# Kernel tuning notes

Hardware: AMD Instinct MI355X
Metric: run time of the kernel (lower is better)

## Reference

```python
import jax, jax.numpy as jnp
import numpy as np

N_NODE = 50000
N_EDGE = 600000
BATCH = 64
IN_DIM = 128
OUT_DIM = 128
ATTN_DIM = 128
N_REL_IDS = 2 * 237 + 1  # 475 relation embedding rows


def setup_inputs() -> dict:
    key = jax.random.key(0)
    ks = jax.random.split(key, 16)
    s = 1.0 / np.sqrt(IN_DIM)
    return {
        "q_sub": jax.random.randint(ks[0], (BATCH,), 0, N_NODE, dtype=jnp.int32),
        "q_rel": jax.random.randint(ks[1], (BATCH,), 0, N_REL_IDS, dtype=jnp.int32),
        "r_idx": jax.random.randint(ks[2], (N_EDGE,), 0, BATCH, dtype=jnp.int32),
        "hidden": jax.random.normal(ks[3], (N_NODE, IN_DIM), dtype=jnp.float32),
        "edge_sub": jax.random.randint(ks[4], (N_EDGE,), 0, N_NODE, dtype=jnp.int32),
        "edge_rel": jax.random.randint(ks[5], (N_EDGE,), 0, N_REL_IDS, dtype=jnp.int32),
        "edge_obj": jax.random.randint(ks[6], (N_EDGE,), 0, N_NODE, dtype=jnp.int32),
        "n_node": N_NODE,
        "rela_embed": jax.random.normal(ks[7], (N_REL_IDS, IN_DIM), dtype=jnp.float32),
        "Ws": jax.random.normal(ks[8], (IN_DIM, ATTN_DIM), dtype=jnp.float32) * s,
        "Wr": jax.random.normal(ks[9], (IN_DIM, ATTN_DIM), dtype=jnp.float32) * s,
        "Wqr_w": jax.random.normal(ks[10], (IN_DIM, ATTN_DIM), dtype=jnp.float32) * s,
        "Wqr_b": jax.random.normal(ks[11], (ATTN_DIM,), dtype=jnp.float32) * s,
        "wa_w": jax.random.normal(ks[12], (ATTN_DIM,), dtype=jnp.float32) * s,
        "wa_b": jax.random.normal(ks[13], (), dtype=jnp.float32) * s,
        "Wh": jax.random.normal(ks[14], (IN_DIM, OUT_DIM), dtype=jnp.float32) * s,
    }


def reference(q_sub, q_rel, r_idx, hidden, edge_sub, edge_rel, edge_obj, n_node,
              rela_embed, Ws, Wr, Wqr_w, Wqr_b, wa_w, wa_b, Wh):
    # gather: per-edge subject hidden state and relation embedding
    hs = hidden[edge_sub]            # [E, in_dim]
    hr = rela_embed[edge_rel]        # [E, in_dim]
    h_qr = rela_embed[q_rel][r_idx]  # [E, in_dim] query-relation embed per edge
    message = hs * hr                # [E, in_dim]
    # attention MLP: sigmoid(w_alpha(relu(Ws hs + Wr hr + Wqr h_qr + b)))
    pre = jax.nn.relu(hs @ Ws + hr @ Wr + h_qr @ Wqr_w + Wqr_b)  # [E, attn]
    alpha = jax.nn.sigmoid(pre @ wa_w + wa_b)                    # [E]
    message = alpha[:, None] * message
    # scatter-add into object node buckets
    message_agg = jax.ops.segment_sum(message, edge_obj, num_segments=n_node)  # [n_node, in_dim]
    # final linear, act = identity (default)
    return message_agg @ Wh
```

## Files before the change

kernel.cpp:

```cpp
#include <hip/hip_runtime.h>

typedef float f32x4 __attribute__((ext_vector_type(4)));
typedef _Float16 f16x8 __attribute__((ext_vector_type(8)));
typedef _Float16 v2h __attribute__((ext_vector_type(2)));
typedef short s16x2 __attribute__((ext_vector_type(2)));

__device__ __forceinline__ float hdot2(v2h a, v2h b, float c) {
#if __has_builtin(__builtin_amdgcn_fdot2)
  return __builtin_amdgcn_fdot2(a, b, c, false);
#else
  return c + (float)a[0] * (float)b[0] + (float)a[1] * (float)b[1];
#endif
}

__device__ __forceinline__ v2h relu2(v2h a) {
#if __has_builtin(__builtin_elementwise_max)
  const v2h z = {(_Float16)0, (_Float16)0};
  return __builtin_elementwise_max(a, z);
#else
  const v2h z = {(_Float16)0, (_Float16)0};
  s16x2 m = a > z;
  s16x2 bits = *(s16x2*)&a;
  s16x2 r = bits & m;
  return *(v2h*)&r;
#endif
}

__global__ __launch_bounds__(256) void conv_wr(
    const float* __restrict__ W0, const float* __restrict__ W1,
    const float* __restrict__ W2, const float* __restrict__ W3,
    _Float16* __restrict__ o0, _Float16* __restrict__ o1,
    _Float16* __restrict__ o2, _Float16* __restrict__ o3,
    const float* __restrict__ rela, _Float16* __restrict__ Rcat, int n_rel) {
  const int id = blockIdx.x * 256 + threadIdx.x;
  if (id < 65536) {
    const int m = id >> 14, e = id & 16383;
    const int k = e >> 7, c = e & 127;
    const float* W = (m == 0) ? W0 : (m == 1) ? W1 : (m == 2) ? W2 : W3;
    _Float16* o = (m == 0) ? o0 : (m == 1) ? o1 : (m == 2) ? o2 : o3;
    o[(k >> 3) * 1024 + c * 8 + (k & 7)] = (_Float16)W[e];
  } else {
    const int rid = id - 65536;
    if (rid < n_rel * 128)
      Rcat[(size_t)(rid >> 7) * 256 + (rid & 127)] = (_Float16)rela[rid];
  }
}

__global__ __launch_bounds__(256) void gemm_rel_dual(
    const _Float16* __restrict__ RcatA, const _Float16* __restrict__ Wrt8,
    const _Float16* __restrict__ Wqrt8, const float* __restrict__ bias,
    _Float16* __restrict__ RcatHi, _Float16* __restrict__ Rwqrt,
    int n_rel, int rel_blocks) {
  __shared__ _Float16 sW[16384];
  const bool second = (int)blockIdx.x >= rel_blocks;
  const int bb = second ? blockIdx.x - rel_blocks : blockIdx.x;
  const _Float16* Wt8 = second ? Wqrt8 : Wrt8;
  for (int i = threadIdx.x; i < 2048; i += 256)
    ((f32x4*)sW)[i] = ((const f32x4*)Wt8)[i];
  __syncthreads();

  const int wv = threadIdx.x >> 6, l = threadIdx.x & 63;
  const int row = bb * 64 + wv * 16 + (l & 15);
  const int kb = (l >> 4) * 8;
  const bool rvalid = row < n_rel;

  f16x8 a[4];
#pragma unroll
  for (int kk = 0; kk < 4; ++kk) {
    f16x8 t = {0, 0, 0, 0, 0, 0, 0, 0};
    if (rvalid) t = *(const f16x8*)(RcatA + (size_t)row * 256 + kb + 32 * kk);
    a[kk] = t;
  }

  f32x4 acc[8];
#pragma unroll
  for (int n = 0; n < 8; ++n) acc[n] = (f32x4){0.f, 0.f, 0.f, 0.f};
#pragma unroll
  for (int n = 0; n < 8; ++n)
#pragma unroll
    for (int kk = 0; kk < 4; ++kk) {
      const int kg = 4 * kk + (l >> 4);
      const f16x8 b = *(const f16x8*)(sW + kg * 1024 + (16 * n + (l & 15)) * 8);
      acc[n] = __builtin_amdgcn_mfma_f32_16x16x32_f16(a[kk], b, acc[n], 0, 0, 0);
    }

  const int orow_base = bb * 64 + wv * 16 + (l >> 4) * 4;
#pragma unroll
  for (int n = 0; n < 8; ++n) {
    const int col = 16 * n + (l & 15);
    const float badd = second ? bias[col] : 0.0f;
#pragma unroll
    for (int r4 = 0; r4 < 4; ++r4) {
      const int orow = orow_base + r4;
      if (orow < n_rel) {
        const float v = acc[n][r4] + badd;
        if (second) Rwqrt[(size_t)orow * 128 + col] = (_Float16)v;
        else        RcatHi[(size_t)orow * 256 + 128 + col] = (_Float16)v;
      }
    }
  }
}

__global__ __launch_bounds__(256) void gemm_hidden(
    const float* __restrict__ hidden, const _Float16* __restrict__ Wst8,
    _Float16* __restrict__ Hcat, int M) {
  __shared__ _Float16 sW[16384];
  for (int i = threadIdx.x; i < 2048; i += 256)
    ((f32x4*)sW)[i] = ((const f32x4*)Wst8)[i];
  __syncthreads();

  const int wv = threadIdx.x >> 6, l = threadIdx.x & 63;
  const int row = blockIdx.x * 64 + wv * 16 + (l & 15);
  const int kb = (l >> 4) * 8;
  const bool rvalid = row < M;

  f16x8 a[4];
#pragma unroll
  for (int kk = 0; kk < 4; ++kk) {
    f16x8 t = {0, 0, 0, 0, 0, 0, 0, 0};
    if (rvalid) {
      const f32x4 lo = *(const f32x4*)(hidden + (size_t)row * 128 + kb + 32 * kk);
      const f32x4 hi = *(const f32x4*)(hidden + (size_t)row * 128 + kb + 32 * kk + 4);
      t[0] = (_Float16)lo[0]; t[1] = (_Float16)lo[1];
      t[2] = (_Float16)lo[2]; t[3] = (_Float16)lo[3];
      t[4] = (_Float16)hi[0]; t[5] = (_Float16)hi[1];
      t[6] = (_Float16)hi[2]; t[7] = (_Float16)hi[3];
      *(f16x8*)(Hcat + (size_t)row * 256 + kb + 32 * kk) = t;
    }
    a[kk] = t;
  }

  f32x4 acc[8];
#pragma unroll
  for (int n = 0; n < 8; ++n) acc[n] = (f32x4){0.f, 0.f, 0.f, 0.f};
#pragma unroll
  for (int n = 0; n < 8; ++n)
#pragma unroll
    for (int kk = 0; kk < 4; ++kk) {
      const int kg = 4 * kk + (l >> 4);
      const f16x8 b = *(const f16x8*)(sW + kg * 1024 + (16 * n + (l & 15)) * 8);
      acc[n] = __builtin_amdgcn_mfma_f32_16x16x32_f16(a[kk], b, acc[n], 0, 0, 0);
    }

  const int orow_base = blockIdx.x * 64 + wv * 16 + (l >> 4) * 4;
#pragma unroll
  for (int n = 0; n < 8; ++n) {
    const int col = 16 * n + (l & 15);
#pragma unroll
    for (int r4 = 0; r4 < 4; ++r4) {
      const int orow = orow_base + r4;
      if (orow < M)
        Hcat[(size_t)orow * 256 + 128 + col] = (_Float16)acc[n][r4];
    }
  }
}

__global__ __launch_bounds__(256) void gemm_final(
    const _Float16* __restrict__ agg, const _Float16* __restrict__ Wht8,
    float* __restrict__ out, int M) {
  __shared__ _Float16 sW[16384];
  for (int i = threadIdx.x; i < 2048; i += 256)
    ((f32x4*)sW)[i] = ((const f32x4*)Wht8)[i];
  __syncthreads();

  const int wv = threadIdx.x >> 6, l = threadIdx.x & 63;
  const int row = blockIdx.x * 64 + wv * 16 + (l & 15);
  const int kb = (l >> 4) * 8;
  const bool rvalid = row < M;

  f16x8 a[4];
#pragma unroll
  for (int kk = 0; kk < 4; ++kk) {
    f16x8 t = {0, 0, 0, 0, 0, 0, 0, 0};
    if (rvalid) t = *(const f16x8*)(agg + (size_t)row * 128 + kb + 32 * kk);
    a[kk] = t;
  }

  f32x4 acc[8];
#pragma unroll
  for (int n = 0; n < 8; ++n) acc[n] = (f32x4){0.f, 0.f, 0.f, 0.f};
#pragma unroll
  for (int n = 0; n < 8; ++n)
#pragma unroll
    for (int kk = 0; kk < 4; ++kk) {
      const int kg = 4 * kk + (l >> 4);
      const f16x8 b = *(const f16x8*)(sW + kg * 1024 + (16 * n + (l & 15)) * 8);
      acc[n] = __builtin_amdgcn_mfma_f32_16x16x32_f16(a[kk], b, acc[n], 0, 0, 0);
    }

  const int orow_base = blockIdx.x * 64 + wv * 16 + (l >> 4) * 4;
#pragma unroll
  for (int n = 0; n < 8; ++n) {
    const int col = 16 * n + (l & 15);
#pragma unroll
    for (int r4 = 0; r4 < 4; ++r4) {
      const int orow = orow_base + r4;
      if (orow < M) out[(size_t)orow * 128 + col] = acc[n][r4];
    }
  }
}

__global__ __launch_bounds__(256) void hist_kernel(const int* __restrict__ edge_obj,
                                                   int* __restrict__ deg, int E) {
  for (int i = blockIdx.x * blockDim.x + threadIdx.x; i < E; i += gridDim.x * blockDim.x)
    atomicAdd(deg + edge_obj[i], 1);
}

__global__ __launch_bounds__(256) void scan_pass1(const int* __restrict__ deg,
                                                  int* __restrict__ bsum, int n) {
  const int b = blockIdx.x, t = threadIdx.x;
  const int i0 = b * 512 + t, i1 = i0 + 256;
  int v = 0;
  if (i0 < n) v += deg[i0];
  if (i1 < n) v += deg[i1];
  __shared__ int s[256];
  s[t] = v;
  __syncthreads();
  for (int o = 128; o > 0; o >>= 1) {
    if (t < o) s[t] += s[t + o];
    __syncthreads();
  }
  if (t == 0) bsum[b] = s[0];
}

__global__ __launch_bounds__(1024) void scan_pass2(const int* __restrict__ bsum,
                                                   int* __restrict__ bbase,
                                                   int* __restrict__ off,
                                                   int nb, int n) {
  const int t = threadIdx.x;
  __shared__ int s[1024];
  const int v = (t < nb) ? bsum[t] : 0;
  s[t] = v;
  __syncthreads();
  for (int o = 1; o < 1024; o <<= 1) {
    const int a = (t >= o) ? s[t - o] : 0;
    __syncthreads();
    s[t] += a;
    __syncthreads();
  }
  if (t < nb) bbase[t] = s[t] - v;
  if (t == 1023) off[n] = s[1023];
}

__global__ __launch_bounds__(256) void scan_pass3(const int* __restrict__ deg,
                                                  const int* __restrict__ bbase,
                                                  int* __restrict__ off,
                                                  int* __restrict__ cursor, int n) {
  const int b = blockIdx.x, t = threadIdx.x;
  const int i0 = b * 512 + t, i1 = i0 + 256;
  const int d0 = (i0 < n) ? deg[i0] : 0;
  const int d1 = (i1 < n) ? deg[i1] : 0;
  __shared__ int s[512];
  s[t] = d0;
  s[t + 256] = d1;
  __syncthreads();
  for (int o = 1; o < 512; o <<= 1) {
    const int a0 = (t >= o) ? s[t - o] : 0;
    const int a1 = (t + 256 >= o) ? s[t + 256 - o] : 0;
    __syncthreads();
    s[t] += a0;
    s[t + 256] += a1;
    __syncthreads();
  }
  const int base = bbase[b];
  if (i0 < n) { const int e = base + s[t] - d0;       off[i0] = e; cursor[i0] = e; }
  if (i1 < n) { const int e = base + s[t + 256] - d1; off[i1] = e; cursor[i1] = e; }
}

__global__ __launch_bounds__(256) void scatter_kernel(
    const int* __restrict__ edge_obj, const int* __restrict__ edge_sub,
    const int* __restrict__ edge_rel, const int* __restrict__ r_idx,
    const int* __restrict__ q_rel, int* __restrict__ cursor,
    int2* __restrict__ ssrq, int E) {
  for (int i = blockIdx.x * blockDim.x + threadIdx.x; i < E; i += gridDim.x * blockDim.x) {
    const int p = atomicAdd(cursor + edge_obj[i], 1);
    ssrq[p] = make_int2(edge_sub[i], (edge_rel[i] << 9) | q_rel[r_idx[i]]);
  }
}

__global__ __launch_bounds__(256) void reduce_f16(
    const int2* __restrict__ ssrq, const int* __restrict__ offs,
    const _Float16* __restrict__ Hcat, const _Float16* __restrict__ Rcat,
    const _Float16* __restrict__ Rwqrt, const float* __restrict__ wa_w,
    const float* __restrict__ wa_b_p, _Float16* __restrict__ agg, int n_node) {
  const int node = (blockIdx.x * blockDim.x + threadIdx.x) >> 6;
  if (node >= n_node) return;
  const int l = threadIdx.x & 63;
  const int g = l >> 4;
  const int d0 = (l & 15) * 8;

  v2h wa2[4];
  {
    const float4 w0 = *(const float4*)(wa_w + d0);
    const float4 w1 = *(const float4*)(wa_w + d0 + 4);
    wa2[0] = (v2h){(_Float16)w0.x, (_Float16)w0.y};
    wa2[1] = (v2h){(_Float16)w0.z, (_Float16)w0.w};
    wa2[2] = (v2h){(_Float16)w1.x, (_Float16)w1.y};
    wa2[3] = (v2h){(_Float16)w1.z, (_Float16)w1.w};
  }
  const float wab = wa_b_p[0];

  const int start = offs[node], end = offs[node + 1];
  v2h acc2[4] = {};

  for (int base = start; base < end; base += 64) {
    const int cnt = min(end - base, 64);
    int s_all = 0, rq_all = 0;
    if (l < cnt) { const int2 sr = ssrq[base + l]; s_all = sr.x; rq_all = sr.y; }
    for (int c = 0; c < cnt; c += 4) {
      const int src = c + g;
      const bool valid = src < cnt;
      const int sv = __shfl(s_all, src);
      const int rqv = __shfl(rq_all, src);
      const int rv = rqv >> 9, qv = rqv & 511;

      f32x4 rw = *(const f32x4*)(Hcat + ((size_t)sv << 8) + 128 + d0);
      f32x4 rr = *(const f32x4*)(Rcat + ((size_t)rv << 8) + 128 + d0);
      f32x4 rq = *(const f32x4*)(Rwqrt + ((size_t)qv << 7) + d0);
      f32x4 rh = *(const f32x4*)(Hcat + ((size_t)sv << 8) + d0);
      f32x4 rg = *(const f32x4*)(Rcat + ((size_t)rv << 8) + d0);
      const v2h* hw = (const v2h*)&rw;
      const v2h* hr_ = (const v2h*)&rr;
      const v2h* hq = (const v2h*)&rq;
      const v2h* hh = (const v2h*)&rh;
      const v2h* hg = (const v2h*)&rg;

      float part = 0.0f;
      v2h prod[4];
#pragma unroll
      for (int i = 0; i < 4; ++i) {
        const v2h pre = relu2(hw[i] + hr_[i] + hq[i]);
        part = hdot2(pre, wa2[i], part);
        prod[i] = hh[i] * hg[i];
      }
      part += __shfl_xor(part, 1);
      part += __shfl_xor(part, 2);
      part += __shfl_xor(part, 4);
      part += __shfl_xor(part, 8);
      const float alpha = valid ? 1.0f / (1.0f + __expf(-(part + wab))) : 0.0f;
      const _Float16 ah = (_Float16)alpha;
      const v2h alpha2 = {ah, ah};
#pragma unroll
      for (int i = 0; i < 4; ++i) acc2[i] += alpha2 * prod[i];
    }
  }

#pragma unroll
  for (int i = 0; i < 4; ++i) {
    unsigned x = *(unsigned*)&acc2[i];
    unsigned y = (unsigned)__shfl_xor((int)x, 16);
    acc2[i] += *(v2h*)&y;
    x = *(unsigned*)&acc2[i];
    y = (unsigned)__shfl_xor((int)x, 32);
    acc2[i] += *(v2h*)&y;
  }
  if (l < 16)
    *(f32x4*)(agg + (size_t)node * 128 + d0) = *(f32x4*)acc2;
}

extern "C" void kernel_launch(void* const* d_in, const int* in_sizes, int n_in,
                              void* d_out, int out_size, void* d_ws, size_t ws_size,
                              hipStream_t stream) {
  const int* q_rel = (const int*)d_in[1];
  const int* r_idx = (const int*)d_in[2];
  const float* hidden = (const float*)d_in[3];
  const int* edge_sub = (const int*)d_in[4];
  const int* edge_rel = (const int*)d_in[5];
  const int* edge_obj = (const int*)d_in[6];
  const float* rela = (const float*)d_in[8];
  const float* Ws = (const float*)d_in[9];
  const float* Wr = (const float*)d_in[10];
  const float* Wqr_w = (const float*)d_in[11];
  const float* Wqr_b = (const float*)d_in[12];
  const float* wa_w = (const float*)d_in[13];
  const float* wa_b = (const float*)d_in[14];
  const float* Wh = (const float*)d_in[15];

  const int E = in_sizes[2];
  const int n_node = in_sizes[3] / 128;
  const int n_rel = in_sizes[8] / 128;
  float* out = (float*)d_out;

  auto al = [](size_t x) { return (x + 511) & ~(size_t)511; };
  char* ws = (char*)d_ws;
  size_t o = 0;
  _Float16* Hcat = (_Float16*)(ws + o);  o += al((size_t)n_node * 256 * 2);
  _Float16* agg  = (_Float16*)(ws + o);  o += al((size_t)n_node * 128 * 2);
  _Float16* Rcat = (_Float16*)(ws + o);  o += al((size_t)n_rel * 256 * 2);
  _Float16* Rwqrt = (_Float16*)(ws + o); o += al((size_t)n_rel * 128 * 2);
  _Float16* Wst8 = (_Float16*)(ws + o);  o += al(16384 * 2);
  _Float16* Wrt8 = (_Float16*)(ws + o);  o += al(16384 * 2);
  _Float16* Wqrt8 = (_Float16*)(ws + o); o += al(16384 * 2);
  _Float16* Wht8 = (_Float16*)(ws + o);  o += al(16384 * 2);
  int* deg = (int*)(ws + o);       o += al((size_t)n_node * 4);
  int* offs = (int*)(ws + o);      o += al((size_t)(n_node + 1) * 4);
  int* curs = (int*)(ws + o);      o += al((size_t)n_node * 4);
  int* bsum = (int*)(ws + o);      o += al(1024 * 4);
  int* bbase = (int*)(ws + o);     o += al(1024 * 4);
  int2* ssrq = (int2*)(ws + o);    o += al((size_t)E * 8);

  (void)hipMemsetAsync(deg, 0, (size_t)n_node * 4, stream);
  hist_kernel<<<dim3(1024), dim3(256), 0, stream>>>(edge_obj, deg, E);
  const int nb = (n_node + 511) / 512;
  scan_pass1<<<dim3(nb), dim3(256), 0, stream>>>(deg, bsum, n_node);
  scan_pass2<<<dim3(1), dim3(1024), 0, stream>>>(bsum, bbase, offs, nb, n_node);
  scan_pass3<<<dim3(nb), dim3(256), 0, stream>>>(deg, bbase, offs, curs, n_node);
  scatter_kernel<<<dim3(1024), dim3(256), 0, stream>>>(
      edge_obj, edge_sub, edge_rel, r_idx, q_rel, curs, ssrq, E);

  const int prep_ids = 65536 + n_rel * 128;
  conv_wr<<<dim3((prep_ids + 255) / 256), dim3(256), 0, stream>>>(
      Ws, Wr, Wqr_w, Wh, Wst8, Wrt8, Wqrt8, Wht8, rela, Rcat, n_rel);

  const int rel_blocks = (n_rel + 63) / 64;
  gemm_rel_dual<<<dim3(rel_blocks * 2), dim3(256), 0, stream>>>(
      Rcat, Wrt8, Wqrt8, Wqr_b, Rcat, Rwqrt, n_rel, rel_blocks);

  const int node_blocks = (n_node + 63) / 64;
  gemm_hidden<<<dim3(node_blocks), dim3(256), 0, stream>>>(hidden, Wst8, Hcat, n_node);

  const int rblocks = (n_node * 64 + 255) / 256;
  reduce_f16<<<dim3(rblocks), dim3(256), 0, stream>>>(
      ssrq, offs, Hcat, Rcat, Rwqrt, wa_w, wa_b, agg, n_node);

  gemm_final<<<dim3(node_blocks), dim3(256), 0, stream>>>(agg, Wht8, out, n_node);
}
```

Measured before the change: 259.3 us.

## Merge sort pipeline into one cooperative kernel and fuse weight prep into GEMMs

Replaces the memset, histogram, three scan passes and scatter with a single cooperative kernel separated by grid-wide syncs. The weight fp32-to-fp16 conversion and relation GEMMs are folded into one prep_gemm launch that converts weights into shared memory per block, and gemm_final converts Wh itself. The aim is to cut the launch count and the intermediate weight buffers. In exchange, every block now redoes the weight conversion, and the grid syncs add latency; the block-level scan now covers at most 256 partial sums instead of 1024.

```diff
diff --git a/kernel.cpp b/kernel.cpp
--- a/kernel.cpp
+++ b/kernel.cpp
@@ -1,4 +1,7 @@
 #include <hip/hip_runtime.h>
+#include <hip/hip_cooperative_groups.h>
+
+namespace cg = cooperative_groups;
 
 typedef float f32x4 __attribute__((ext_vector_type(4)));
 typedef _Float16 f16x8 __attribute__((ext_vector_type(8)));
@@ -26,49 +29,131 @@
 #endif
 }
 
-__global__ __launch_bounds__(256) void conv_wr(
-    const float* __restrict__ W0, const float* __restrict__ W1,
-    const float* __restrict__ W2, const float* __restrict__ W3,
-    _Float16* __restrict__ o0, _Float16* __restrict__ o1,
-    _Float16* __restrict__ o2, _Float16* __restrict__ o3,
-    const float* __restrict__ rela, _Float16* __restrict__ Rcat, int n_rel) {
-  const int id = blockIdx.x * 256 + threadIdx.x;
-  if (id < 65536) {
-    const int m = id >> 14, e = id & 16383;
-    const int k = e >> 7, c = e & 127;
-    const float* W = (m == 0) ? W0 : (m == 1) ? W1 : (m == 2) ? W2 : W3;
-    _Float16* o = (m == 0) ? o0 : (m == 1) ? o1 : (m == 2) ? o2 : o3;
-    o[(k >> 3) * 1024 + c * 8 + (k & 7)] = (_Float16)W[e];
+__global__ __launch_bounds__(256, 4) void sort_coop(
+    const int* __restrict__ edge_obj, const int* __restrict__ edge_sub,
+    const int* __restrict__ edge_rel, const int* __restrict__ r_idx,
+    const int* __restrict__ q_rel, int* deg, int* bsum, int* bbase,
+    int* offs, int* curs, int2* ssrq, int E, int n, int nb) {
+  cg::grid_group grid = cg::this_grid();
+  __shared__ int s[512];
+  const int tid = blockIdx.x * 256 + threadIdx.x;
+  const int nthr = gridDim.x * 256;
+  const int t = threadIdx.x;
+  const int b = blockIdx.x;
+
+  for (int i = tid; i < n; i += nthr) deg[i] = 0;
+  grid.sync();
+
+  for (int i = tid; i < E; i += nthr) atomicAdd(&deg[edge_obj[i]], 1);
+  grid.sync();
+
+  if (b < nb) {
+    const int i0 = b * 512 + t, i1 = i0 + 256;
+    int v = 0;
+    if (i0 < n) v += deg[i0];
+    if (i1 < n) v += deg[i1];
+    s[t] = v;
+    __syncthreads();
+    for (int o = 128; o > 0; o >>= 1) {
+      if (t < o) s[t] += s[t + o];
+      __syncthreads();
+    }
+    if (t == 0) bsum[b] = s[0];
+  }
+  grid.sync();
+
+  if (b == 0) {
+    const int v = (t < nb) ? bsum[t] : 0;
+    s[t] = v;
+    __syncthreads();
+    for (int o = 1; o < 256; o <<= 1) {
+      const int a = (t >= o) ? s[t - o] : 0;
+      __syncthreads();
+      s[t] += a;
+      __syncthreads();
+    }
+    if (t < nb) bbase[t] = s[t] - v;
+    if (t == 255) offs[n] = s[255];
+  }
+  grid.sync();
+
+  if (b < nb) {
+    const int i0 = b * 512 + t, i1 = i0 + 256;
+    const int d0 = (i0 < n) ? deg[i0] : 0;
+    const int d1 = (i1 < n) ? deg[i1] : 0;
+    s[t] = d0;
+    s[t + 256] = d1;
+    __syncthreads();
+    for (int o = 1; o < 512; o <<= 1) {
+      const int a0 = (t >= o) ? s[t - o] : 0;
+      const int a1 = (t + 256 >= o) ? s[t + 256 - o] : 0;
+      __syncthreads();
+      s[t] += a0;
+      s[t + 256] += a1;
+      __syncthreads();
+    }
+    const int base = bbase[b];
+    if (i0 < n) { const int e = base + s[t] - d0;       offs[i0] = e; curs[i0] = e; }
+    if (i1 < n) { const int e = base + s[t + 256] - d1; offs[i1] = e; curs[i1] = e; }
+  }
+  grid.sync();
+
+  for (int i = tid; i < E; i += nthr) {
+    const int p = atomicAdd(&curs[edge_obj[i]], 1);
+    ssrq[p] = make_int2(edge_sub[i], (edge_rel[i] << 9) | q_rel[r_idx[i]]);
+  }
+}
+
+__global__ __launch_bounds__(256) void prep_gemm(
+    const float* __restrict__ hidden, const float* __restrict__ rela,
+    const float* __restrict__ Ws, const float* __restrict__ Wr,
+    const float* __restrict__ Wqr, const float* __restrict__ Wqr_b,
+    _Float16* __restrict__ Hcat, _Float16* __restrict__ Rcat,
+    _Float16* __restrict__ Rwqrt, int n_node, int n_rel,
+    int hid_blocks, int rel_blocks) {
+  __shared__ _Float16 sW[16384];
+  const int bidx = blockIdx.x;
+  const float* A;
+  const float* W;
+  const float* bias = nullptr;
+  _Float16* Lo = nullptr;
+  _Float16* Chi;
+  int M, bb, ldc, coff;
+  if (bidx < hid_blocks) {
+    bb = bidx; A = hidden; W = Ws; Lo = Hcat; Chi = Hcat;
+    M = n_node; ldc = 256; coff = 128;
+  } else if (bidx < hid_blocks + rel_blocks) {
+    bb = bidx - hid_blocks; A = rela; W = Wr; Lo = Rcat; Chi = Rcat;
+    M = n_rel; ldc = 256; coff = 128;
   } else {
-    const int rid = id - 65536;
-    if (rid < n_rel * 128)
-      Rcat[(size_t)(rid >> 7) * 256 + (rid & 127)] = (_Float16)rela[rid];
-  }
-}
-
-__global__ __launch_bounds__(256) void gemm_rel_dual(
-    const _Float16* __restrict__ RcatA, const _Float16* __restrict__ Wrt8,
-    const _Float16* __restrict__ Wqrt8, const float* __restrict__ bias,
-    _Float16* __restrict__ RcatHi, _Float16* __restrict__ Rwqrt,
-    int n_rel, int rel_blocks) {
-  __shared__ _Float16 sW[16384];
-  const bool second = (int)blockIdx.x >= rel_blocks;
-  const int bb = second ? blockIdx.x - rel_blocks : blockIdx.x;
-  const _Float16* Wt8 = second ? Wqrt8 : Wrt8;
-  for (int i = threadIdx.x; i < 2048; i += 256)
-    ((f32x4*)sW)[i] = ((const f32x4*)Wt8)[i];
+    bb = bidx - hid_blocks - rel_blocks; A = rela; W = Wqr; Chi = Rwqrt;
+    bias = Wqr_b; M = n_rel; ldc = 128; coff = 0;
+  }
+
+  for (int i = threadIdx.x; i < 16384; i += 256) {
+    const int k = i >> 7, c = i & 127;
+    sW[(k >> 3) * 1024 + c * 8 + (k & 7)] = (_Float16)W[i];
+  }
   __syncthreads();
 
   const int wv = threadIdx.x >> 6, l = threadIdx.x & 63;
   const int row = bb * 64 + wv * 16 + (l & 15);
   const int kb = (l >> 4) * 8;
-  const bool rvalid = row < n_rel;
+  const bool rvalid = row < M;
 
   f16x8 a[4];
 #pragma unroll
   for (int kk = 0; kk < 4; ++kk) {
     f16x8 t = {0, 0, 0, 0, 0, 0, 0, 0};
-    if (rvalid) t = *(const f16x8*)(RcatA + (size_t)row * 256 + kb + 32 * kk);
+    if (rvalid) {
+      const f32x4 lo = *(const f32x4*)(A + (size_t)row * 128 + kb + 32 * kk);
+      const f32x4 hi = *(const f32x4*)(A + (size_t)row * 128 + kb + 32 * kk + 4);
+      t[0] = (_Float16)lo[0]; t[1] = (_Float16)lo[1];
+      t[2] = (_Float16)lo[2]; t[3] = (_Float16)lo[3];
+      t[4] = (_Float16)hi[0]; t[5] = (_Float16)hi[1];
+      t[6] = (_Float16)hi[2]; t[7] = (_Float16)hi[3];
+      if (Lo) *(f16x8*)(Lo + (size_t)row * 256 + kb + 32 * kk) = t;
+    }
     a[kk] = t;
   }
 
@@ -80,33 +165,32 @@
 #pragma unroll
     for (int kk = 0; kk < 4; ++kk) {
       const int kg = 4 * kk + (l >> 4);
-      const f16x8 b = *(const f16x8*)(sW + kg * 1024 + (16 * n + (l & 15)) * 8);
-      acc[n] = __builtin_amdgcn_mfma_f32_16x16x32_f16(a[kk], b, acc[n], 0, 0, 0);
+      const f16x8 bfrag = *(const f16x8*)(sW + kg * 1024 + (16 * n + (l & 15)) * 8);
+      acc[n] = __builtin_amdgcn_mfma_f32_16x16x32_f16(a[kk], bfrag, acc[n], 0, 0, 0);
     }
 
   const int orow_base = bb * 64 + wv * 16 + (l >> 4) * 4;
 #pragma unroll
   for (int n = 0; n < 8; ++n) {
     const int col = 16 * n + (l & 15);
-    const float badd = second ? bias[col] : 0.0f;
+    const float badd = bias ? bias[col] : 0.0f;
 #pragma unroll
     for (int r4 = 0; r4 < 4; ++r4) {
       const int orow = orow_base + r4;
-      if (orow < n_rel) {
-        const float v = acc[n][r4] + badd;
-        if (second) Rwqrt[(size_t)orow * 128 + col] = (_Float16)v;
-        else        RcatHi[(size_t)orow * 256 + 128 + col] = (_Float16)v;
-      }
-    }
-  }
-}
-
-__global__ __launch_bounds__(256) void gemm_hidden(
-    const float* __restrict__ hidden, const _Float16* __restrict__ Wst8,
-    _Float16* __restrict__ Hcat, int M) {
+      if (orow < M)
+        Chi[(size_t)orow * ldc + coff + col] = (_Float16)(acc[n][r4] + badd);
+    }
+  }
+}
+
+__global__ __launch_bounds__(256) void gemm_final(
+    const _Float16* __restrict__ agg, const float* __restrict__ Wh,
+    float* __restrict__ out, int M) {
   __shared__ _Float16 sW[16384];
-  for (int i = threadIdx.x; i < 2048; i += 256)
-    ((f32x4*)sW)[i] = ((const f32x4*)Wst8)[i];
+  for (int i = threadIdx.x; i < 16384; i += 256) {
+    const int k = i >> 7, c = i & 127;
+    sW[(k >> 3) * 1024 + c * 8 + (k & 7)] = (_Float16)Wh[i];
+  }
   __syncthreads();
 
   const int wv = threadIdx.x >> 6, l = threadIdx.x & 63;
@@ -118,15 +202,7 @@
 #pragma unroll
   for (int kk = 0; kk < 4; ++kk) {
     f16x8 t = {0, 0, 0, 0, 0, 0, 0, 0};
-    if (rvalid) {
-      const f32x4 lo = *(const f32x4*)(hidden + (size_t)row * 128 + kb + 32 * kk);
-      const f32x4 hi = *(const f32x4*)(hidden + (size_t)row * 128 + kb + 32 * kk + 4);
-      t[0] = (_Float16)lo[0]; t[1] = (_Float16)lo[1];
-      t[2] = (_Float16)lo[2]; t[3] = (_Float16)lo[3];
-      t[4] = (_Float16)hi[0]; t[5] = (_Float16)hi[1];
-      t[6] = (_Float16)hi[2]; t[7] = (_Float16)hi[3];
-      *(f16x8*)(Hcat + (size_t)row * 256 + kb + 32 * kk) = t;
-    }
+    if (rvalid) t = *(const f16x8*)(agg + (size_t)row * 128 + kb + 32 * kk);
     a[kk] = t;
   }
 
@@ -138,54 +214,8 @@
 #pragma unroll
     for (int kk = 0; kk < 4; ++kk) {
       const int kg = 4 * kk + (l >> 4);
-      const f16x8 b = *(const f16x8*)(sW + kg * 1024 + (16 * n + (l & 15)) * 8);
-      acc[n] = __builtin_amdgcn_mfma_f32_16x16x32_f16(a[kk], b, acc[n], 0, 0, 0);
-    }
-
-  const int orow_base = blockIdx.x * 64 + wv * 16 + (l >> 4) * 4;
-#pragma unroll
-  for (int n = 0; n < 8; ++n) {
-    const int col = 16 * n + (l & 15);
-#pragma unroll
-    for (int r4 = 0; r4 < 4; ++r4) {
-      const int orow = orow_base + r4;
-      if (orow < M)
-        Hcat[(size_t)orow * 256 + 128 + col] = (_Float16)acc[n][r4];
-    }
-  }
-}
-
-__global__ __launch_bounds__(256) void gemm_final(
-    const _Float16* __restrict__ agg, const _Float16* __restrict__ Wht8,
-    float* __restrict__ out, int M) {
-  __shared__ _Float16 sW[16384];
-  for (int i = threadIdx.x; i < 2048; i += 256)
-    ((f32x4*)sW)[i] = ((const f32x4*)Wht8)[i];
-  __syncthreads();
-
-  const int wv = threadIdx.x >> 6, l = threadIdx.x & 63;
-  const int row = blockIdx.x * 64 + wv * 16 + (l & 15);
-  const int kb = (l >> 4) * 8;
-  const bool rvalid = row < M;
-
-  f16x8 a[4];
-#pragma unroll
-  for (int kk = 0; kk < 4; ++kk) {
-    f16x8 t = {0, 0, 0, 0, 0, 0, 0, 0};
-    if (rvalid) t = *(const f16x8*)(agg + (size_t)row * 128 + kb + 32 * kk);
-    a[kk] = t;
-  }
-
-  f32x4 acc[8];
-#pragma unroll
-  for (int n = 0; n < 8; ++n) acc[n] = (f32x4){0.f, 0.f, 0.f, 0.f};
-#pragma unroll
-  for (int n = 0; n < 8; ++n)
-#pragma unroll
-    for (int kk = 0; kk < 4; ++kk) {
-      const int kg = 4 * kk + (l >> 4);
-      const f16x8 b = *(const f16x8*)(sW + kg * 1024 + (16 * n + (l & 15)) * 8);
-      acc[n] = __builtin_amdgcn_mfma_f32_16x16x32_f16(a[kk], b, acc[n], 0, 0, 0);
+      const f16x8 bfrag = *(const f16x8*)(sW + kg * 1024 + (16 * n + (l & 15)) * 8);
+      acc[n] = __builtin_amdgcn_mfma_f32_16x16x32_f16(a[kk], bfrag, acc[n], 0, 0, 0);
     }
 
   const int orow_base = blockIdx.x * 64 + wv * 16 + (l >> 4) * 4;
@@ -197,84 +227,6 @@
       const int orow = orow_base + r4;
       if (orow < M) out[(size_t)orow * 128 + col] = acc[n][r4];
     }
-  }
-}
-
-__global__ __launch_bounds__(256) void hist_kernel(const int* __restrict__ edge_obj,
-                                                   int* __restrict__ deg, int E) {
-  for (int i = blockIdx.x * blockDim.x + threadIdx.x; i < E; i += gridDim.x * blockDim.x)
-    atomicAdd(deg + edge_obj[i], 1);
-}
-
-__global__ __launch_bounds__(256) void scan_pass1(const int* __restrict__ deg,
-                                                  int* __restrict__ bsum, int n) {
-  const int b = blockIdx.x, t = threadIdx.x;
-  const int i0 = b * 512 + t, i1 = i0 + 256;
-  int v = 0;
-  if (i0 < n) v += deg[i0];
-  if (i1 < n) v += deg[i1];
-  __shared__ int s[256];
-  s[t] = v;
-  __syncthreads();
-  for (int o = 128; o > 0; o >>= 1) {
-    if (t < o) s[t] += s[t + o];
-    __syncthreads();
-  }
-  if (t == 0) bsum[b] = s[0];
-}
-
-__global__ __launch_bounds__(1024) void scan_pass2(const int* __restrict__ bsum,
-                                                   int* __restrict__ bbase,
-                                                   int* __restrict__ off,
-                                                   int nb, int n) {
-  const int t = threadIdx.x;
-  __shared__ int s[1024];
-  const int v = (t < nb) ? bsum[t] : 0;
-  s[t] = v;
-  __syncthreads();
-  for (int o = 1; o < 1024; o <<= 1) {
-    const int a = (t >= o) ? s[t - o] : 0;
-    __syncthreads();
-    s[t] += a;
-    __syncthreads();
-  }
-  if (t < nb) bbase[t] = s[t] - v;
-  if (t == 1023) off[n] = s[1023];
-}
-
-__global__ __launch_bounds__(256) void scan_pass3(const int* __restrict__ deg,
-                                                  const int* __restrict__ bbase,
-                                                  int* __restrict__ off,
-                                                  int* __restrict__ cursor, int n) {
-  const int b = blockIdx.x, t = threadIdx.x;
-  const int i0 = b * 512 + t, i1 = i0 + 256;
-  const int d0 = (i0 < n) ? deg[i0] : 0;
-  const int d1 = (i1 < n) ? deg[i1] : 0;
-  __shared__ int s[512];
-  s[t] = d0;
-  s[t + 256] = d1;
-  __syncthreads();
-  for (int o = 1; o < 512; o <<= 1) {
-    const int a0 = (t >= o) ? s[t - o] : 0;
-    const int a1 = (t + 256 >= o) ? s[t + 256 - o] : 0;
-    __syncthreads();
-    s[t] += a0;
-    s[t + 256] += a1;
-    __syncthreads();
-  }
-  const int base = bbase[b];
-  if (i0 < n) { const int e = base + s[t] - d0;       off[i0] = e; cursor[i0] = e; }
-  if (i1 < n) { const int e = base + s[t + 256] - d1; off[i1] = e; cursor[i1] = e; }
-}
-
-__global__ __launch_bounds__(256) void scatter_kernel(
-    const int* __restrict__ edge_obj, const int* __restrict__ edge_sub,
-    const int* __restrict__ edge_rel, const int* __restrict__ r_idx,
-    const int* __restrict__ q_rel, int* __restrict__ cursor,
-    int2* __restrict__ ssrq, int E) {
-  for (int i = blockIdx.x * blockDim.x + threadIdx.x; i < E; i += gridDim.x * blockDim.x) {
-    const int p = atomicAdd(cursor + edge_obj[i], 1);
-    ssrq[p] = make_int2(edge_sub[i], (edge_rel[i] << 9) | q_rel[r_idx[i]]);
   }
 }
 
@@ -376,8 +328,8 @@
   const float* wa_b = (const float*)d_in[14];
   const float* Wh = (const float*)d_in[15];
 
-  const int E = in_sizes[2];
-  const int n_node = in_sizes[3] / 128;
+  int E = in_sizes[2];
+  int n_node = in_sizes[3] / 128;
   const int n_rel = in_sizes[8] / 128;
   float* out = (float*)d_out;
 
@@ -388,10 +340,6 @@
   _Float16* agg  = (_Float16*)(ws + o);  o += al((size_t)n_node * 128 * 2);
   _Float16* Rcat = (_Float16*)(ws + o);  o += al((size_t)n_rel * 256 * 2);
   _Float16* Rwqrt = (_Float16*)(ws + o); o += al((size_t)n_rel * 128 * 2);
-  _Float16* Wst8 = (_Float16*)(ws + o);  o += al(16384 * 2);
-  _Float16* Wrt8 = (_Float16*)(ws + o);  o += al(16384 * 2);
-  _Float16* Wqrt8 = (_Float16*)(ws + o); o += al(16384 * 2);
-  _Float16* Wht8 = (_Float16*)(ws + o);  o += al(16384 * 2);
   int* deg = (int*)(ws + o);       o += al((size_t)n_node * 4);
   int* offs = (int*)(ws + o);      o += al((size_t)(n_node + 1) * 4);
   int* curs = (int*)(ws + o);      o += al((size_t)n_node * 4);
@@ -399,29 +347,26 @@
   int* bbase = (int*)(ws + o);     o += al(1024 * 4);
   int2* ssrq = (int2*)(ws + o);    o += al((size_t)E * 8);
 
-  (void)hipMemsetAsync(deg, 0, (size_t)n_node * 4, stream);
-  hist_kernel<<<dim3(1024), dim3(256), 0, stream>>>(edge_obj, deg, E);
-  const int nb = (n_node + 511) / 512;
-  scan_pass1<<<dim3(nb), dim3(256), 0, stream>>>(deg, bsum, n_node);
-  scan_pass2<<<dim3(1), dim3(1024), 0, stream>>>(bsum, bbase, offs, nb, n_node);
-  scan_pass3<<<dim3(nb), dim3(256), 0, stream>>>(deg, bbase, offs, curs, n_node);
-  scatter_kernel<<<dim3(1024), dim3(256), 0, stream>>>(
-      edge_obj, edge_sub, edge_rel, r_idx, q_rel, curs, ssrq, E);
-
-  const int prep_ids = 65536 + n_rel * 128;
-  conv_wr<<<dim3((prep_ids + 255) / 256), dim3(256), 0, stream>>>(
-      Ws, Wr, Wqr_w, Wh, Wst8, Wrt8, Wqrt8, Wht8, rela, Rcat, n_rel);
-
+  int nb = (n_node + 511) / 512;
+  {
+    void* args[] = {(void*)&edge_obj, (void*)&edge_sub, (void*)&edge_rel,
+                    (void*)&r_idx,    (void*)&q_rel,    (void*)&deg,
+                    (void*)&bsum,     (void*)&bbase,    (void*)&offs,
+                    (void*)&curs,     (void*)&ssrq,     (void*)&E,
+                    (void*)&n_node,   (void*)&nb};
+    (void)hipLaunchCooperativeKernel((void*)sort_coop, dim3(1024), dim3(256),
+                                     args, 0, stream);
+  }
+
+  const int hid_blocks = (n_node + 63) / 64;
   const int rel_blocks = (n_rel + 63) / 64;
-  gemm_rel_dual<<<dim3(rel_blocks * 2), dim3(256), 0, stream>>>(
-      Rcat, Wrt8, Wqrt8, Wqr_b, Rcat, Rwqrt, n_rel, rel_blocks);
-
-  const int node_blocks = (n_node + 63) / 64;
-  gemm_hidden<<<dim3(node_blocks), dim3(256), 0, stream>>>(hidden, Wst8, Hcat, n_node);
+  prep_gemm<<<dim3(hid_blocks + 2 * rel_blocks), dim3(256), 0, stream>>>(
+      hidden, rela, Ws, Wr, Wqr_w, Wqr_b, Hcat, Rcat, Rwqrt,
+      n_node, n_rel, hid_blocks, rel_blocks);
 
   const int rblocks = (n_node * 64 + 255) / 256;
   reduce_f16<<<dim3(rblocks), dim3(256), 0, stream>>>(
       ssrq, offs, Hcat, Rcat, Rwqrt, wa_w, wa_b, agg, n_node);
 
-  gemm_final<<<dim3(node_blocks), dim3(256), 0, stream>>>(agg, Wht8, out, n_node);
-}
+  gemm_final<<<dim3(hid_blocks), dim3(256), 0, stream>>>(agg, Wh, out, n_node);
+}
```

New measurement: 796.2 us. 3.07x slower.
